# Kernel tuning notes

Hardware: AMD Instinct MI355X
Metric: run time of the kernel (lower is better)

Reference implementation:

```python
import jax, jax.numpy as jnp
import numpy as np

# Model dims
T = 256        # seq_length (timesteps)
B = 16384      # batch
IN = 1024      # hardcoded input feature dim of LILinearCell
C = 10         # n_classes
# norse LIParameters defaults
DT = 1e-3
TAU_SYN_INV = 200.0
TAU_MEM_INV = 100.0
V_LEAK = 0.0


def setup_inputs() -> dict:
    key = jax.random.key(0)
    kx, kw = jax.random.split(key)
    x = jax.random.normal(kx, (B, IN), dtype=jnp.float32)
    # LILinearCell weight init: randn(out,in) * sqrt(2/in)
    W = jax.random.normal(kw, (C, IN), dtype=jnp.float32) * np.float32(np.sqrt(2.0 / IN))
    return {"x": x, "W": W}


def reference(x, W):
    # uses_ts=False: the same x feeds every timestep, so the synaptic input
    # current x @ W^T is constant across the scan.
    xW = x @ W.T  # [B, C]

    def step(state, _):
        v, i = state
        # norse li_step:
        i_jump = i + xW
        v_new = v + DT * TAU_MEM_INV * ((V_LEAK - v) + i_jump)
        i_new = i_jump - DT * TAU_SYN_INV * i_jump
        return (v_new, i_new), v_new

    v0 = jnp.full((x.shape[0], W.shape[0]), V_LEAK, dtype=x.dtype)
    i0 = jnp.zeros((x.shape[0], W.shape[0]), dtype=x.dtype)
    _, voltages = jax.lax.scan(step, (v0, i0), None, length=T)
    return voltages  # [T, B, C]
```

## Files before the change

### kernel.cpp

```cpp
#include <hip/hip_runtime.h>

#define T_STEPS 256
#define B_ROWS  16384
#define IN_DIM  1024
#define C_CLS   10

typedef float vfloat4 __attribute__((ext_vector_type(4)));

__global__ __launch_bounds__(256) void gemv_kernel(
    const float4* __restrict__ x4,
    const float4* __restrict__ W4,
    float* __restrict__ xw)
{
    const int tid  = threadIdx.x;
    const int wave = tid >> 6;
    const int lane = tid & 63;
    const int sub  = lane >> 4;
    const int ql   = lane & 15;
    const int row  = blockIdx.x * 16 + wave * 4 + sub;

    float acc[C_CLS];
#pragma unroll
    for (int c = 0; c < C_CLS; ++c) acc[c] = 0.0f;

    const float4* __restrict__ xrow = x4 + (size_t)row * 256;

#pragma unroll 4
    for (int p = 0; p < 16; ++p) {
        float4 xv = xrow[p * 16 + ql];
#pragma unroll
        for (int c = 0; c < C_CLS; ++c) {
            float4 w = W4[c * 256 + p * 16 + ql];
            acc[c] = fmaf(xv.x, w.x,
                     fmaf(xv.y, w.y,
                     fmaf(xv.z, w.z,
                     fmaf(xv.w, w.w, acc[c]))));
        }
    }

#pragma unroll
    for (int c = 0; c < C_CLS; ++c) {
        float v = acc[c];
#pragma unroll
        for (int off = 8; off >= 1; off >>= 1)
            v += __shfl_xor(v, off, 64);
        acc[c] = v;
    }

    if (ql == 0) {
#pragma unroll
        for (int c = 0; c < C_CLS; ++c)
            xw[row * C_CLS + c] = acc[c];
    }
}

#define T_CHUNK 16
__global__ __launch_bounds__(256) void expand_kernel(
    const float4* __restrict__ xw4,
    float4* __restrict__ out4)
{
    const int SLICE4 = (B_ROWS * C_CLS) / 4;
    const int NR     = SLICE4 / 256;

    const int rblk = blockIdx.x % NR;
    const int tblk = blockIdx.x / NR;
    const int r4   = rblk * 256 + threadIdx.x;
    const int t0   = tblk * T_CHUNK;

    const float L9 = -0.15200309344504995f;
    const float L8 = -0.32192809488736235f;

    float4 v = xw4[r4];
    float p9 = exp2f((float)(t0 + 1) * L9);
    float p8 = exp2f((float)(t0 + 1) * L8);

    float4* dst = out4 + (size_t)t0 * SLICE4 + r4;
#pragma unroll
    for (int i = 0; i < T_CHUNK; ++i) {
        float coef = fmaf(-9.0f, p9, fmaf(4.0f, p8, 5.0f));
        vfloat4 o;
        o.x = v.x * coef; o.y = v.y * coef; o.z = v.z * coef; o.w = v.w * coef;
        __builtin_nontemporal_store(o, (vfloat4*)dst);
        dst += SLICE4;
        p9 *= 0.9f;
        p8 *= 0.8f;
    }
}

extern "C" void kernel_launch(void* const* d_in, const int* in_sizes, int n_in,
                              void* d_out, int out_size, void* d_ws, size_t ws_size,
                              hipStream_t stream) {
    const float* x = (const float*)d_in[0];
    const float* W = (const float*)d_in[1];
    float* out = (float*)d_out;
    float* xw  = (float*)d_ws;

    gemv_kernel<<<B_ROWS / 16, 256, 0, stream>>>(
        (const float4*)x, (const float4*)W, xw);

    expand_kernel<<<(T_STEPS / T_CHUNK) * ((B_ROWS * C_CLS) / 4 / 256), 256, 0, stream>>>(
        (const float4*)xw, (float4*)out);
}
```

Baseline: 233.1 us.

## Reuse W registers across four rows per wave in GEMV and stream x nontemporally

```diff
diff --git a/kernel.cpp b/kernel.cpp
--- a/kernel.cpp
+++ b/kernel.cpp
@@ -8,7 +8,7 @@
 typedef float vfloat4 __attribute__((ext_vector_type(4)));
 
 __global__ __launch_bounds__(256) void gemv_kernel(
-    const float4* __restrict__ x4,
+    const vfloat4* __restrict__ x4,
     const float4* __restrict__ W4,
     float* __restrict__ xw)
 {
@@ -16,41 +16,50 @@
     const int wave = tid >> 6;
     const int lane = tid & 63;
     const int sub  = lane >> 4;
-    const int ql   = lane & 15;
-    const int row  = blockIdx.x * 16 + wave * 4 + sub;
+    const int row_base = blockIdx.x * 16 + wave * 4;
 
-    float acc[C_CLS];
+    float acc[4][C_CLS];
 #pragma unroll
-    for (int c = 0; c < C_CLS; ++c) acc[c] = 0.0f;
+    for (int r = 0; r < 4; ++r)
+#pragma unroll
+        for (int c = 0; c < C_CLS; ++c) acc[r][c] = 0.0f;
 
-    const float4* __restrict__ xrow = x4 + (size_t)row * 256;
+#pragma unroll
+    for (int p = 0; p < 4; ++p) {
+        float4 w[C_CLS];
+#pragma unroll
+        for (int c = 0; c < C_CLS; ++c)
+            w[c] = W4[c * 256 + p * 64 + lane];
 
-#pragma unroll 4
-    for (int p = 0; p < 16; ++p) {
-        float4 xv = xrow[p * 16 + ql];
 #pragma unroll
-        for (int c = 0; c < C_CLS; ++c) {
-            float4 w = W4[c * 256 + p * 16 + ql];
-            acc[c] = fmaf(xv.x, w.x,
-                     fmaf(xv.y, w.y,
-                     fmaf(xv.z, w.z,
-                     fmaf(xv.w, w.w, acc[c]))));
+        for (int r = 0; r < 4; ++r) {
+            vfloat4 xv = __builtin_nontemporal_load(
+                x4 + (size_t)(row_base + r) * 256 + p * 64 + lane);
+#pragma unroll
+            for (int c = 0; c < C_CLS; ++c) {
+                acc[r][c] = fmaf(xv.x, w[c].x,
+                            fmaf(xv.y, w[c].y,
+                            fmaf(xv.z, w[c].z,
+                            fmaf(xv.w, w[c].w, acc[r][c]))));
+            }
         }
     }
 
 #pragma unroll
     for (int c = 0; c < C_CLS; ++c) {
-        float v = acc[c];
 #pragma unroll
-        for (int off = 8; off >= 1; off >>= 1)
-            v += __shfl_xor(v, off, 64);
-        acc[c] = v;
-    }
-
-    if (ql == 0) {
-#pragma unroll
-        for (int c = 0; c < C_CLS; ++c)
-            xw[row * C_CLS + c] = acc[c];
+        for (int r = 0; r < 4; ++r) {
+            acc[r][c] += __shfl_xor(acc[r][c], 32, 64);
+            acc[r][c] += __shfl_xor(acc[r][c], 16, 64);
+        }
+        float p = (sub < 2) ? (sub == 0 ? acc[0][c] : acc[1][c])
+                            : (sub == 2 ? acc[2][c] : acc[3][c]);
+        p += __shfl_xor(p, 8, 64);
+        p += __shfl_xor(p, 4, 64);
+        p += __shfl_xor(p, 2, 64);
+        p += __shfl_xor(p, 1, 64);
+        if ((lane & 15) == 0)
+            xw[(row_base + sub) * C_CLS + c] = p;
     }
 }
 
@@ -96,7 +105,7 @@
     float* xw  = (float*)d_ws;
 
     gemv_kernel<<<B_ROWS / 16, 256, 0, stream>>>(
-        (const float4*)x, (const float4*)W, xw);
+        (const vfloat4*)x, (const float4*)W, xw);
 
     expand_kernel<<<(T_STEPS / T_CHUNK) * ((B_ROWS * C_CLS) / 4 / 256), 256, 0, stream>>>(
         (const float4*)xw, (float4*)out);
```

New measurement: 218.8 us. -6.1%, faster.
